# Optimization experiments

Measured on AMD Instinct MI355X. Metric: run time of the kernel, lower is better.

The kernel has to match this reference:

```python
import jax, jax.numpy as jnp
import numpy as np
import math

D = 300      # input_size
H = 5        # gat heads
NLAYERS = 2  # txt_gat_layer == img_gat_layer
N, L, K = 64, 1024, 64
E_TXT, E_IMG = 2048, 512


def _gat(x, edge_index, W, att_src, att_dst, bias):
    """PyG GATConv, concat=False (head mean), no self loops, eval mode (no dropout).
    x: (n, D); edge_index: (2, E); W: (D, H, D); att_*: (H, D); bias: (D,)."""
    n = x.shape[0]
    h = jnp.einsum('ld,dhe->lhe', x, W)                    # (n, H, D)
    src, dst = edge_index[0], edge_index[1]
    a_src = jnp.sum(h * att_src, axis=-1)                  # (n, H)
    a_dst = jnp.sum(h * att_dst, axis=-1)                  # (n, H)
    e = jax.nn.leaky_relu(a_src[src] + a_dst[dst], 0.2)    # (E, H)
    m = jax.ops.segment_max(e, dst, num_segments=n)        # per-target max
    m = jnp.where(jnp.isfinite(m), m, 0.0)                 # nodes w/o in-edges
    p = jnp.exp(e - m[dst])
    denom = jax.ops.segment_sum(p, dst, num_segments=n)
    alpha = p / (denom[dst] + 1e-16)                       # (E, H)
    out = jax.ops.segment_sum(alpha[:, :, None] * h[src], dst, num_segments=n)
    return out.mean(axis=1) + bias                         # (n, D)


def _layer_norm(x, g, b):
    mu = jnp.mean(x, axis=-1, keepdims=True)
    var = jnp.mean((x - mu) ** 2, axis=-1, keepdims=True)
    return (x - mu) / jnp.sqrt(var + 1e-5) * g + b


def _forward(t2, v2, score, edge_index, gnn_mask, key_padding_mask, np_mask,
             img_edge_index, txt_W, txt_att_src, txt_att_dst, txt_bias,
             img_W, img_att_src, img_att_dst, img_bias,
             w1, b1, w2, b2, ln_g, ln_b, lam=1.0):
    scale = 1.0 / jnp.sqrt(jnp.asarray(D, t2.dtype))
    q1 = jnp.einsum('nld,nkd->nlk', t2, v2) * scale        # (N, L, K)
    c = jnp.sum(score * t2, axis=1, keepdims=True)         # (N, 1, D)
    pa_token = t2 @ w1 + b1                                # (N, L)
    pa_token = jnp.where(key_padding_mask, -jnp.inf, pa_token)

    gat_txt = jax.vmap(_gat, in_axes=(0, 0, None, None, None, None))
    tnp = t2
    for i in range(NLAYERS):
        g = gat_txt(tnp, edge_index, txt_W[i], txt_att_src[i], txt_att_dst[i], txt_bias[i])
        g = jnp.where(gnn_mask[:, None, None], 0.0, g)     # masked graph -> zeros
        tnp = _layer_norm(jax.nn.relu(g), ln_g, ln_b)

    gat_img = jax.vmap(_gat, in_axes=(0, None, None, None, None, None))
    v3 = v2
    for i in range(NLAYERS):
        g = gat_img(v3, img_edge_index, img_W[i], img_att_src[i], img_att_dst[i], img_bias[i])
        v3 = _layer_norm(jax.nn.relu(g), ln_g, ln_b)

    tnp = jnp.concatenate([tnp, c], axis=1)                # (N, L+1, D)
    q2 = jnp.einsum('nld,nkd->nlk', tnp, v3) * scale       # (N, L+1, K)
    pa_np = tnp @ w2 + b2                                  # (N, L+1)
    pa_np = jnp.where(np_mask, -jnp.inf, pa_np)
    pa_np = jax.nn.softmax(pa_np * lam, axis=1)
    pa_tok = jax.nn.softmax(pa_token * lam, axis=1)
    a1 = jnp.sum(q1 * pa_tok[:, :, None], axis=1)          # (N, K)
    a2 = jnp.sum(q2 * pa_np[:, :, None], axis=1)           # (N, K)
    return jnp.concatenate([a1, a2], axis=1)               # (N, 2K)


def setup_inputs() -> dict:
    key = jax.random.key(0)
    ks = jax.random.split(key, 24)
    ws = 1.0 / math.sqrt(D)
    return {
        't2': jax.random.normal(ks[0], (N, L, D), jnp.float32),
        'v2': jax.random.normal(ks[1], (N, K, D), jnp.float32),
        'score': jax.random.uniform(ks[2], (N, L, D), jnp.float32),
        'edge_index': jax.random.randint(ks[3], (N, 2, E_TXT), 0, L),
        'gnn_mask': jnp.zeros((N,), bool),
        'key_padding_mask': jax.random.bernoulli(ks[4], 0.1, (N, L)),
        'np_mask': jax.random.bernoulli(ks[5], 0.1, (N, L + 1)),
        'img_edge_index': jax.random.randint(ks[6], (2, E_IMG), 0, K),
        'txt_W': jax.random.normal(ks[7], (NLAYERS, D, H, D), jnp.float32) * ws,
        'txt_att_src': jax.random.normal(ks[8], (NLAYERS, H, D), jnp.float32) * 0.1,
        'txt_att_dst': jax.random.normal(ks[9], (NLAYERS, H, D), jnp.float32) * 0.1,
        'txt_bias': jnp.zeros((NLAYERS, D), jnp.float32),
        'img_W': jax.random.normal(ks[10], (NLAYERS, D, H, D), jnp.float32) * ws,
        'img_att_src': jax.random.normal(ks[11], (NLAYERS, H, D), jnp.float32) * 0.1,
        'img_att_dst': jax.random.normal(ks[12], (NLAYERS, H, D), jnp.float32) * 0.1,
        'img_bias': jnp.zeros((NLAYERS, D), jnp.float32),
        'w1': jax.random.normal(ks[13], (D,), jnp.float32) * ws,
        'b1': jnp.zeros((), jnp.float32),
        'w2': jax.random.normal(ks[14], (D,), jnp.float32) * ws,
        'b2': jnp.zeros((), jnp.float32),
        'ln_g': jnp.ones((D,), jnp.float32),
        'ln_b': jnp.zeros((D,), jnp.float32),
    }


def reference(t2, v2, score, edge_index, gnn_mask, key_padding_mask, np_mask,
              img_edge_index, txt_W, txt_att_src, txt_att_dst, txt_bias,
              img_W, img_att_src, img_att_dst, img_bias,
              w1, b1, w2, b2, ln_g, ln_b):
    return _forward(t2, v2, score, edge_index, gnn_mask, key_padding_mask, np_mask,
                    img_edge_index, txt_W, txt_att_src, txt_att_dst, txt_bias,
                    img_W, img_att_src, img_att_dst, img_bias,
                    w1, b1, w2, b2, ln_g, ln_b)
```

## Files before the change

### kernel.cpp

```cpp
#include <hip/hip_runtime.h>
#include <hip/hip_bf16.h>
#include <math.h>

typedef __hip_bfloat16 bf16;
__device__ __forceinline__ float toF(float v){ return v; }
__device__ __forceinline__ float toF(bf16 v){ return __bfloat162float(v); }
__device__ __forceinline__ bf16 f2bf(float v){ return __float2bfloat16(v); }

#define D_    300
#define H_    5
#define NB    64
#define LL    1024
#define KK    64
#define ETXT  2048
#define EIMG  512
#define MAXDEG 128
#define KP    320
#define NP    1536

typedef __attribute__((ext_vector_type(8))) short short8;
typedef __attribute__((ext_vector_type(4))) float f32x4;

__device__ __forceinline__ int read_mask(const void* p, int i, int mode) {
  switch (mode) {
    case 1: return ((const unsigned short*)p)[i] != 0;
    case 2: return ((const unsigned char*)p)[i] != 0;
    case 3: { const unsigned int* w = (const unsigned int*)p;
              return (w[2*i] | w[2*i+1]) != 0; }
    default: return ((const unsigned int*)p)[i] != 0;
  }
}

__global__ void k_detect(const unsigned int* __restrict__ w, int nwords,
                         int* __restrict__ mode) {
  __shared__ unsigned int se[256], so[256];
  unsigned int oe = 0, oo = 0;
  for (int i = threadIdx.x; i < nwords; i += 256) {
    unsigned int v = w[i];
    if (i & 1) oo |= v; else oe |= v;
  }
  se[threadIdx.x] = oe; so[threadIdx.x] = oo;
  __syncthreads();
  for (int s = 128; s; s >>= 1) {
    if (threadIdx.x < s) { se[threadIdx.x] |= se[threadIdx.x+s]; so[threadIdx.x] |= so[threadIdx.x+s]; }
    __syncthreads();
  }
  if (threadIdx.x == 0) {
    unsigned int O = se[0] | so[0];
    int m = 0;
    if (O == 0u) m = 0;
    else if ((O & 0xFFFFu) == 0x3F80u) m = 1;
    else if ((O >> 16) == 0x3F80u && (O & 0xFFFFu) == 0u) m = 0;
    else if ((O >> 16) == 0x3FF0u) m = 3;
    else if (O <= 1u) m = (so[0] == 0u && se[0] != 0u) ? 3 : 0;
    else if ((O & 0xFEFEFEFEu) == 0u) m = 2;
    mode[0] = m;
  }
}

__global__ __launch_bounds__(256) void k_csr(const int* __restrict__ edges, int estride,
                                             int E, int nodes,
                                             int* __restrict__ rowptr, int rstride,
                                             int* __restrict__ col, int cstride) {
  int g = blockIdx.x, tid = threadIdx.x;
  __shared__ int cnt[1025];
  __shared__ int psum[257];
  const int* src = edges + (size_t)g * estride;
  const int* dst = src + E;
  for (int i = tid; i <= nodes; i += 256) cnt[i] = 0;
  __syncthreads();
  for (int e = tid; e < E; e += 256) atomicAdd(&cnt[dst[e]], 1);
  __syncthreads();
  int base = tid * 4;
  int loc = 0;
#pragma unroll
  for (int i = 0; i < 4; ++i) { int idx = base + i; if (idx < nodes) loc += cnt[idx]; }
  psum[tid + 1] = loc;
  if (tid == 0) psum[0] = 0;
  __syncthreads();
  if (tid == 0) { for (int i = 1; i <= 256; ++i) psum[i] += psum[i - 1]; }
  __syncthreads();
  int run = psum[tid];
  int starts[4];
#pragma unroll
  for (int i = 0; i < 4; ++i) {
    int idx = base + i;
    if (idx < nodes) { int c = cnt[idx]; starts[i] = run; run += c; }
  }
  __syncthreads();
#pragma unroll
  for (int i = 0; i < 4; ++i) {
    int idx = base + i;
    if (idx < nodes) { cnt[idx] = starts[i]; rowptr[(size_t)g * rstride + idx] = starts[i]; }
  }
  if (tid == 0) rowptr[(size_t)g * rstride + nodes] = E;
  __syncthreads();
  for (int e = tid; e < E; e += 256) {
    int pos = atomicAdd(&cnt[dst[e]], 1);
    col[(size_t)g * cstride + pos] = src[e];
  }
}

__global__ void k_c(const float* __restrict__ t2, const float* __restrict__ score,
                    float* __restrict__ c) {
  int n = blockIdx.x;
  int d = blockIdx.y * 128 + threadIdx.x;
  if (d >= D_) return;
  const float* tp = t2 + (size_t)n * LL * D_ + d;
  const float* sp = score + (size_t)n * LL * D_ + d;
  float acc = 0.f;
  for (int l = 0; l < LL; ++l)
    acc += tp[(size_t)l * D_] * sp[(size_t)l * D_];
  c[n * D_ + d] = acc;
}

__device__ __forceinline__ float clamp_logit(float v) {
  if (!(v > -1e30f)) v = -1e30f;
  if (v > 1e30f) v = 1e30f;
  return v;
}

__global__ void k_logits_tok(const float* __restrict__ x, const float* __restrict__ w,
                             const float* __restrict__ b, const void* __restrict__ mask,
                             const int* __restrict__ mmode,
                             float* __restrict__ logits, int rows) {
  int row = blockIdx.x * blockDim.y + threadIdx.y;
  if (row >= rows) return;
  int lane = threadIdx.x;
  const float* xp = x + (size_t)row * D_;
  float acc = 0.f;
  for (int d = lane; d < D_; d += 64) acc += xp[d] * w[d];
#pragma unroll
  for (int off = 32; off; off >>= 1) acc += __shfl_down(acc, off);
  if (lane == 0) {
    float v = clamp_logit(acc + b[0]);
    if (read_mask(mask, row, mmode[0])) v = -INFINITY;
    logits[row] = v;
  }
}

__global__ void k_logits_np(const bf16* __restrict__ X, const float* __restrict__ c,
                            const float* __restrict__ w, const float* __restrict__ b,
                            const void* __restrict__ mask, const int* __restrict__ mmode,
                            float* __restrict__ logits) {
  int row = blockIdx.x * blockDim.y + threadIdx.y;
  if (row >= NB * (LL + 1)) return;
  int n = row / (LL + 1), l = row % (LL + 1);
  int lane = threadIdx.x;
  float acc = 0.f;
  if (l < LL) {
    const bf16* xp = X + ((size_t)n * LL + l) * D_;
    for (int d = lane; d < D_; d += 64) acc += toF(xp[d]) * w[d];
  } else {
    const float* cp = c + n * D_;
    for (int d = lane; d < D_; d += 64) acc += cp[d] * w[d];
  }
#pragma unroll
  for (int off = 32; off; off >>= 1) acc += __shfl_down(acc, off);
  if (lane == 0) {
    float v = clamp_logit(acc + b[0]);
    if (read_mask(mask, row, mmode[0])) v = -INFINITY;
    logits[row] = v;
  }
}

__global__ __launch_bounds__(256) void k_soft_u1(const float* __restrict__ logits,
                                                 const float* __restrict__ t2,
                                                 float* __restrict__ u1) {
  int n = blockIdx.x, tid = threadIdx.x;
  __shared__ float w[LL];
  __shared__ float red[4];
  __shared__ float stat;
  float m = -INFINITY;
  for (int l = tid; l < LL; l += 256) { float v = logits[n * LL + l]; w[l] = v; m = fmaxf(m, v); }
#pragma unroll
  for (int off = 32; off; off >>= 1) m = fmaxf(m, __shfl_down(m, off));
  if ((tid & 63) == 0) red[tid >> 6] = m;
  __syncthreads();
  if (tid == 0) stat = fmaxf(fmaxf(red[0], red[1]), fmaxf(red[2], red[3]));
  __syncthreads();
  float M = stat;
  if (!(M > -INFINITY && M < INFINITY)) M = 0.f;
  float s = 0.f;
  for (int l = tid; l < LL; l += 256) { float p = __expf(w[l] - M); w[l] = p; s += p; }
#pragma unroll
  for (int off = 32; off; off >>= 1) s += __shfl_down(s, off);
  __syncthreads();
  if ((tid & 63) == 0) red[tid >> 6] = s;
  __syncthreads();
  if (tid == 0) stat = red[0] + red[1] + red[2] + red[3];
  __syncthreads();
  float inv = (stat > 0.f) ? 1.f / stat : 0.f;
  for (int d = tid; d < D_; d += 256) {
    float acc = 0.f;
    const float* tp = t2 + (size_t)n * LL * D_ + d;
    for (int l = 0; l < LL; ++l) acc += w[l] * tp[(size_t)l * D_];
    u1[n * D_ + d] = acc * inv;
  }
}

__global__ __launch_bounds__(256) void k_soft_u2(const float* __restrict__ logits,
                                                 const bf16* __restrict__ X,
                                                 const float* __restrict__ c,
                                                 float* __restrict__ u2) {
  int n = blockIdx.x, tid = threadIdx.x;
  __shared__ float w[LL + 1];
  __shared__ float red[4];
  __shared__ float stat;
  float m = -INFINITY;
  for (int l = tid; l < LL + 1; l += 256) { float v = logits[n * (LL + 1) + l]; w[l] = v; m = fmaxf(m, v); }
#pragma unroll
  for (int off = 32; off; off >>= 1) m = fmaxf(m, __shfl_down(m, off));
  if ((tid & 63) == 0) red[tid >> 6] = m;
  __syncthreads();
  if (tid == 0) stat = fmaxf(fmaxf(red[0], red[1]), fmaxf(red[2], red[3]));
  __syncthreads();
  float M = stat;
  if (!(M > -INFINITY && M < INFINITY)) M = 0.f;
  float s = 0.f;
  for (int l = tid; l < LL + 1; l += 256) { float p = __expf(w[l] - M); w[l] = p; s += p; }
#pragma unroll
  for (int off = 32; off; off >>= 1) s += __shfl_down(s, off);
  __syncthreads();
  if ((tid & 63) == 0) red[tid >> 6] = s;
  __syncthreads();
  if (tid == 0) stat = red[0] + red[1] + red[2] + red[3];
  __syncthreads();
  float inv = (stat > 0.f) ? 1.f / stat : 0.f;
  for (int d = tid; d < D_; d += 256) {
    float acc = 0.f;
    const bf16* xp = X + (size_t)n * LL * D_ + d;
    for (int l = 0; l < LL; ++l) acc += w[l] * toF(xp[(size_t)l * D_]);
    acc += w[LL] * c[n * D_ + d];
    u2[n * D_ + d] = acc * inv;
  }
}

__global__ void k_wvec(const float* __restrict__ W, const float* __restrict__ att_src,
                       const float* __restrict__ att_dst, float* __restrict__ wsrc,
                       float* __restrict__ wdst) {
  int idx = blockIdx.x * blockDim.x + threadIdx.x;
  if (idx >= 2 * H_ * D_) return;
  int s = idx / (H_ * D_);
  int r = idx % (H_ * D_);
  int h = r / D_, d = r % D_;
  const float* att = (s ? att_dst : att_src) + h * D_;
  const float* Wp = W + (size_t)d * H_ * D_ + h * D_;
  float acc = 0.f;
  for (int e = 0; e < D_; ++e) acc += Wp[e] * att[e];
  (s ? wdst : wsrc)[h * D_ + d] = acc;
}

template <typename T>
__global__ void k_asrc(const T* __restrict__ x, const float* __restrict__ wsrc,
                       const float* __restrict__ wdst, float* __restrict__ a_src,
                       float* __restrict__ a_dst, int rows) {
  int row = blockIdx.x * blockDim.y + threadIdx.y;
  if (row >= rows) return;
  int lane = threadIdx.x;
  const T* xp = x + (size_t)row * D_;
  float xr[5];
#pragma unroll
  for (int i = 0; i < 5; ++i) { int d = lane + 64 * i; xr[i] = (d < D_) ? toF(xp[d]) : 0.f; }
#pragma unroll
  for (int hh = 0; hh < H_; ++hh) {
    float as = 0.f, ad = 0.f;
#pragma unroll
    for (int i = 0; i < 5; ++i) {
      int d = lane + 64 * i;
      if (d < D_) { as += xr[i] * wsrc[hh * D_ + d]; ad += xr[i] * wdst[hh * D_ + d]; }
    }
#pragma unroll
    for (int off = 32; off; off >>= 1) { as += __shfl_down(as, off); ad += __shfl_down(ad, off); }
    if (lane == 0) { a_src[(size_t)row * H_ + hh] = as; a_dst[(size_t)row * H_ + hh] = ad; }
  }
}

template <typename T>
__global__ void k_packA(const T* __restrict__ src, bf16* __restrict__ Ap, int M) {
  int idx = blockIdx.x * 256 + threadIdx.x;
  if (idx >= M * KP) return;
  int m = idx / KP, k = idx - m * KP;
  Ap[idx] = (k < D_) ? f2bf(toF(src[(size_t)m * D_ + k])) : f2bf(0.f);
}

__global__ void k_packB(const float* __restrict__ B, bf16* __restrict__ Bp) {
  int idx = blockIdx.x * 256 + threadIdx.x;
  if (idx >= NP * KP) return;
  int j = idx / KP, k = idx - j * KP;
  float v = (k < D_ && j < H_ * D_) ? B[(size_t)k * (H_ * D_) + j] : 0.f;
  Bp[idx] = f2bf(v);
}

__global__ __launch_bounds__(256) void k_gemm_mfma(const bf16* __restrict__ Ap,
                                                   const bf16* __restrict__ Bp,
                                                   bf16* __restrict__ C, int M) {
  __shared__ short As[128][40];
  __shared__ short Bs[128][40];
  int m0 = blockIdx.x * 128, n0 = blockIdx.y * 128;
  int tid = threadIdx.x;
  int wave = tid >> 6, lane = tid & 63;
  int wr = (wave >> 1) * 64, wc = (wave & 1) * 64;
  f32x4 acc[4][4] = {};
  for (int k0 = 0; k0 < KP; k0 += 32) {
#pragma unroll
    for (int cc = 0; cc < 2; ++cc) {
      int c = tid + cc * 256;
      int m = c >> 2, ko = (c & 3) << 3;
      int row = m0 + m; if (row >= M) row = M - 1;
      *(uint4*)&As[m][ko] = *(const uint4*)(Ap + (size_t)row * KP + k0 + ko);
    }
#pragma unroll
    for (int cc = 0; cc < 2; ++cc) {
      int c = tid + cc * 256;
      int n = c >> 2, ko = (c & 3) << 3;
      *(uint4*)&Bs[n][ko] = *(const uint4*)(Bp + (size_t)(n0 + n) * KP + k0 + ko);
    }
    __syncthreads();
    int kq = (lane >> 4) << 3;
    short8 af[4], bfr[4];
#pragma unroll
    for (int i = 0; i < 4; ++i) af[i]  = *(const short8*)&As[wr + i * 16 + (lane & 15)][kq];
#pragma unroll
    for (int j = 0; j < 4; ++j) bfr[j] = *(const short8*)&Bs[wc + j * 16 + (lane & 15)][kq];
#pragma unroll
    for (int i = 0; i < 4; ++i)
#pragma unroll
      for (int j = 0; j < 4; ++j)
        acc[i][j] = __builtin_amdgcn_mfma_f32_16x16x32_bf16(af[i], bfr[j], acc[i][j], 0, 0, 0);
    __syncthreads();
  }
  int cl = lane & 15, rq = (lane >> 4) << 2;
#pragma unroll
  for (int i = 0; i < 4; ++i) {
#pragma unroll
    for (int j = 0; j < 4; ++j) {
      int col = n0 + wc + j * 16 + cl;
#pragma unroll
      for (int r = 0; r < 4; ++r) {
        int row = m0 + wr + i * 16 + rq + r;
        if (row < M) C[(size_t)row * NP + col] = f2bf(acc[i][j][r]);
      }
    }
  }
}

__global__ __launch_bounds__(256) void k_agg_ln(
    const bf16* __restrict__ h, const float* __restrict__ a_src, const float* __restrict__ a_dst,
    const int* __restrict__ rowptr, int rstride,
    const int* __restrict__ col, int cstride,
    int nodes, int lbpg, int swz, int gs,
    const void* __restrict__ gmask, const int* __restrict__ mmode, int g_off,
    const float* __restrict__ bias, const float* __restrict__ g_ln, const float* __restrict__ b_ln,
    bf16* __restrict__ xout) {
  int b = blockIdx.x;
  int wv = threadIdx.x >> 6, lane = threadIdx.x & 63;
  int g, nb;
  if (swz) { int j = b >> 3; g = (b & 7) + ((j >> lbpg) << 3); nb = j & ((1 << lbpg) - 1); }
  else     { g = b >> lbpg; nb = b & ((1 << lbpg) - 1); }
  int node = (nb << 2) + wv;
  if (g >= gs || node >= nodes) return;
  int gg = g_off + g;
  const int* rp = rowptr + (size_t)gg * rstride;
  int r0 = rp[node];
  int deg = rp[node + 1] - r0;
  if (deg > MAXDEG) deg = MAXDEG;
  const int* cp = col + (size_t)gg * cstride + r0;
  int row0 = g * nodes;
  const float* adr = a_dst + (size_t)(row0 + node) * H_;
  float ad[H_];
#pragma unroll
  for (int hh = 0; hh < H_; ++hh) ad[hh] = adr[hh];
  int d0 = deg < 64 ? deg : 64;
  int s0 = 0; float l0[H_];
  if (lane < d0) {
    s0 = cp[lane];
    const float* ap = a_src + (size_t)(row0 + s0) * H_;
#pragma unroll
    for (int hh = 0; hh < H_; ++hh) { float v = ap[hh] + ad[hh]; l0[hh] = v > 0.f ? v : 0.2f * v; }
  } else {
#pragma unroll
    for (int hh = 0; hh < H_; ++hh) l0[hh] = -INFINITY;
  }
  bool two = deg > 64;
  int s1 = 0; float l1[H_];
#pragma unroll
  for (int hh = 0; hh < H_; ++hh) l1[hh] = -INFINITY;
  if (two && lane < deg - 64) {
    s1 = cp[64 + lane];
    const float* ap = a_src + (size_t)(row0 + s1) * H_;
#pragma unroll
    for (int hh = 0; hh < H_; ++hh) { float v = ap[hh] + ad[hh]; l1[hh] = v > 0.f ? v : 0.2f * v; }
  }
  float al0[H_], al1[H_];
#pragma unroll
  for (int hh = 0; hh < H_; ++hh) {
    float m = two ? fmaxf(l0[hh], l1[hh]) : l0[hh];
    for (int off = 1; off < deg && off < 64; off <<= 1) m = fmaxf(m, __shfl_xor(m, off));
    m = __shfl(m, 0);
    float e0 = (lane < d0) ? __expf(l0[hh] - m) : 0.f;
    float e1 = (two && lane < deg - 64) ? __expf(l1[hh] - m) : 0.f;
    float s = e0 + e1;
    for (int off = 1; off < deg && off < 64; off <<= 1) s += __shfl_xor(s, off);
    s = __shfl(s, 0);
    float inv = 1.f / (s + 1e-16f);
    al0[hh] = e0 * inv;
    al1[hh] = e1 * inv;
  }
  float acc[3][2] = {};
  const char* hb = (const char*)h;
  for (int i = 0; i < deg; ++i) {
    int si; float aw[H_];
    if (i < 64) {
      si = __shfl(s0, i);
#pragma unroll
      for (int hh = 0; hh < H_; ++hh) aw[hh] = __shfl(al0[hh], i);
    } else {
      si = __shfl(s1, i - 64);
#pragma unroll
      for (int hh = 0; hh < H_; ++hh) aw[hh] = __shfl(al1[hh], i - 64);
    }
    const char* rb = hb + (size_t)(row0 + si) * (NP * 2);
#pragma unroll
    for (int t = 0; t < 3; ++t) {
      int d2 = lane + 64 * t;
      if (d2 < 150) {
#pragma unroll
        for (int hh = 0; hh < H_; ++hh) {
          unsigned int u = *(const unsigned int*)(rb + hh * (D_ * 2) + d2 * 4);
          float lo = __uint_as_float(u << 16);
          float hi = __uint_as_float(u & 0xFFFF0000u);
          acc[t][0] += aw[hh] * lo;
          acc[t][1] += aw[hh] * hi;
        }
      }
    }
  }
  int msk = gmask ? read_mask(gmask, gg, mmode[0]) : 0;
  float y[3][2];
  float ps = 0.f, pq = 0.f;
#pragma unroll
  for (int t = 0; t < 3; ++t) {
    int d2 = lane + 64 * t;
    float y0 = 0.f, y1 = 0.f;
    if (d2 < 150) {
      float2 bb = *(const float2*)&bias[d2 * 2];
      y0 = acc[t][0] * (1.f / H_) + bb.x;
      y1 = acc[t][1] * (1.f / H_) + bb.y;
      if (msk) { y0 = 0.f; y1 = 0.f; }
      y0 = fmaxf(y0, 0.f); y1 = fmaxf(y1, 0.f);
      ps += y0 + y1; pq += y0 * y0 + y1 * y1;
    }
    y[t][0] = y0; y[t][1] = y1;
  }
#pragma unroll
  for (int off = 1; off < 64; off <<= 1) { ps += __shfl_xor(ps, off); pq += __shfl_xor(pq, off); }
  float mu = ps * (1.f / 300.f);
  float var = pq * (1.f / 300.f) - mu * mu;
  var = fmaxf(var, 0.f);
  float rstd = rsqrtf(var + 1e-5f);
  char* orow = (char*)(xout + (size_t)(row0 + node) * D_);
#pragma unroll
  for (int t = 0; t < 3; ++t) {
    int d2 = lane + 64 * t;
    if (d2 < 150) {
      float2 gv = *(const float2*)&g_ln[d2 * 2];
      float2 bv = *(const float2*)&b_ln[d2 * 2];
      float o0 = (y[t][0] - mu) * rstd * gv.x + bv.x;
      float o1 = (y[t][1] - mu) * rstd * gv.y + bv.y;
      bf16 c0 = f2bf(o0), c1 = f2bf(o1);
      unsigned int u = ((unsigned int)*(unsigned short*)&c1 << 16) | (unsigned int)*(unsigned short*)&c0;
      *(unsigned int*)(orow + d2 * 4) = u;
    }
  }
}

__global__ void k_out(const float* __restrict__ u1, const float* __restrict__ u2,
                      const float* __restrict__ v2, const bf16* __restrict__ v3,
                      float* __restrict__ out) {
  int idx = blockIdx.x * blockDim.y + threadIdx.y;
  if (idx >= NB * KK) return;
  int n = idx / KK, k = idx - n * KK;
  int lane = threadIdx.x;
  const float* ap = v2 + (size_t)idx * D_;
  const bf16* bp = v3 + (size_t)idx * D_;
  const float* u1p = u1 + n * D_;
  const float* u2p = u2 + n * D_;
  float a1 = 0.f, a2 = 0.f;
  for (int d = lane; d < D_; d += 64) { a1 += u1p[d] * ap[d]; a2 += u2p[d] * toF(bp[d]); }
#pragma unroll
  for (int off = 32; off; off >>= 1) { a1 += __shfl_down(a1, off); a2 += __shfl_down(a2, off); }
  if (lane == 0) {
    const float scale = 0.05773502691896258f;
    out[(size_t)n * 2 * KK + k] = a1 * scale;
    out[(size_t)n * 2 * KK + KK + k] = a2 * scale;
  }
}

extern "C" void kernel_launch(void* const* d_in, const int* in_sizes, int n_in,
                              void* d_out, int out_size, void* d_ws, size_t ws_size,
                              hipStream_t stream) {
  const float* t2    = (const float*)d_in[0];
  const float* v2    = (const float*)d_in[1];
  const float* score = (const float*)d_in[2];
  const int*   eidx  = (const int*)d_in[3];
  const void*  gmask = d_in[4];
  const void*  kpm   = d_in[5];
  const void*  npm   = d_in[6];
  const int*   iedge = (const int*)d_in[7];
  const float* txtW  = (const float*)d_in[8];
  const float* txtAs = (const float*)d_in[9];
  const float* txtAd = (const float*)d_in[10];
  const float* txtB  = (const float*)d_in[11];
  const float* imgW  = (const float*)d_in[12];
  const float* imgAs = (const float*)d_in[13];
  const float* imgAd = (const float*)d_in[14];
  const float* imgB  = (const float*)d_in[15];
  const float* w1    = (const float*)d_in[16];
  const float* b1    = (const float*)d_in[17];
  const float* w2    = (const float*)d_in[18];
  const float* b2    = (const float*)d_in[19];
  const float* lng   = (const float*)d_in[20];
  const float* lnb   = (const float*)d_in[21];
  float* out = (float*)d_out;

  char* ws = (char*)d_ws;
  size_t off = 0;
  auto alloc = [&](size_t bytes) -> char* {
    char* p = ws + off;
    off += (bytes + 511) & ~(size_t)511;
    return p;
  };
  int*   mmode = (int*)alloc(64);
  float* c    = (float*)alloc((size_t)NB * D_ * 4);
  float* u1   = (float*)alloc((size_t)NB * D_ * 4);
  float* u2   = (float*)alloc((size_t)NB * D_ * 4);
  float* lg1  = (float*)alloc((size_t)NB * LL * 4);
  float* lg2  = (float*)alloc((size_t)NB * (LL + 1) * 4);
  float* wsrc = (float*)alloc((size_t)H_ * D_ * 4);
  float* wdst = (float*)alloc((size_t)H_ * D_ * 4);
  float* asrc = (float*)alloc((size_t)NB * LL * H_ * 4);
  float* adst = (float*)alloc((size_t)NB * LL * H_ * 4);
  int*   trp  = (int*)alloc((size_t)NB * (LL + 1) * 4);
  int*   tcol = (int*)alloc((size_t)NB * ETXT * 4);
  int*   irp  = (int*)alloc((size_t)(KK + 1) * 4);
  int*   icol = (int*)alloc((size_t)EIMG * 4);
  bf16* X  = (bf16*)alloc((size_t)NB * LL * D_ * 2);
  bf16* V  = (bf16*)alloc((size_t)NB * KK * D_ * 2);
  bf16* Bp = (bf16*)alloc((size_t)NP * KP * 2);
  size_t havail = (ws_size > off) ? (ws_size - off) : 0;
  char* hstart = ws + off;
  size_t per_g_txt = (size_t)LL * (KP + NP) * 2;
  int cg = (int)(havail / per_g_txt);
  if (cg < 1) cg = 1;
  if (cg > NB) cg = NB;
  size_t per_g_img = (size_t)KK * (KP + NP) * 2;
  int cgi = (int)(havail / per_g_img);
  if (cgi < 1) cgi = 1;
  if (cgi > NB) cgi = NB;

  dim3 b64x4(64, 4);

  k_detect<<<1, 256, 0, stream>>>((const unsigned int*)kpm, NB * LL / 4, mmode);

  k_csr<<<NB, 256, 0, stream>>>(eidx, 2 * ETXT, ETXT, LL, trp, LL + 1, tcol, ETXT);
  k_csr<<<1, 256, 0, stream>>>(iedge, 0, EIMG, KK, irp, 0, icol, 0);

  k_c<<<dim3(NB, 3), 128, 0, stream>>>(t2, score, c);
  k_logits_tok<<<(NB * LL + 3) / 4, b64x4, 0, stream>>>(t2, w1, b1, kpm, mmode, lg1, NB * LL);
  k_soft_u1<<<NB, 256, 0, stream>>>(lg1, t2, u1);

  {
    bf16* Ap   = (bf16*)hstart;
    bf16* hbuf = (bf16*)(hstart + (size_t)cg * LL * KP * 2);
    for (int layer = 0; layer < 2; ++layer) {
      const float* W = txtW + (size_t)layer * D_ * H_ * D_;
      k_packB<<<(NP * KP + 255) / 256, 256, 0, stream>>>(W, Bp);
      k_wvec<<<(2 * H_ * D_ + 255) / 256, 256, 0, stream>>>(
          W, txtAs + layer * H_ * D_, txtAd + layer * H_ * D_, wsrc, wdst);
      for (int g0 = 0; g0 < NB; g0 += cg) {
        int gs = (cg < NB - g0) ? cg : (NB - g0);
        int M = gs * LL;
        bf16* Xout = X + (size_t)g0 * LL * D_;
        if (layer == 0) {
          const float* Xin = t2 + (size_t)g0 * LL * D_;
          k_packA<float><<<(M * KP + 255) / 256, 256, 0, stream>>>(Xin, Ap, M);
          k_asrc<float><<<(M + 3) / 4, b64x4, 0, stream>>>(Xin, wsrc, wdst, asrc, adst, M);
        } else {
          const bf16* Xin = X + (size_t)g0 * LL * D_;
          k_packA<bf16><<<(M * KP + 255) / 256, 256, 0, stream>>>(Xin, Ap, M);
          k_asrc<bf16><<<(M + 3) / 4, b64x4, 0, stream>>>(Xin, wsrc, wdst, asrc, adst, M);
        }
        k_gemm_mfma<<<dim3((M + 127) / 128, NP / 128), 256, 0, stream>>>(Ap, Bp, hbuf, M);
        int swz = (gs % 8 == 0);
        k_agg_ln<<<gs * (LL / 4), 256, 0, stream>>>(hbuf, asrc, adst, trp, LL + 1, tcol, ETXT,
                                                    LL, 8, swz, gs, gmask, mmode, g0,
                                                    txtB + layer * D_, lng, lnb, Xout);
      }
    }
  }

  {
    bf16* Ap   = (bf16*)hstart;
    bf16* hbuf = (bf16*)(hstart + (size_t)cgi * KK * KP * 2);
    for (int layer = 0; layer < 2; ++layer) {
      const float* W = imgW + (size_t)layer * D_ * H_ * D_;
      k_packB<<<(NP * KP + 255) / 256, 256, 0, stream>>>(W, Bp);
      k_wvec<<<(2 * H_ * D_ + 255) / 256, 256, 0, stream>>>(
          W, imgAs + layer * H_ * D_, imgAd + layer * H_ * D_, wsrc, wdst);
      for (int g0 = 0; g0 < NB; g0 += cgi) {
        int gs = (cgi < NB - g0) ? cgi : (NB - g0);
        int M = gs * KK;
        bf16* Vout = V + (size_t)g0 * KK * D_;
        if (layer == 0) {
          const float* Vin = v2 + (size_t)g0 * KK * D_;
          k_packA<float><<<(M * KP + 255) / 256, 256, 0, stream>>>(Vin, Ap, M);
          k_asrc<float><<<(M + 3) / 4, b64x4, 0, stream>>>(Vin, wsrc, wdst, asrc, adst, M);
        } else {
          const bf16* Vin = V + (size_t)g0 * KK * D_;
          k_packA<bf16><<<(M * KP + 255) / 256, 256, 0, stream>>>(Vin, Ap, M);
          k_asrc<bf16><<<(M + 3) / 4, b64x4, 0, stream>>>(Vin, wsrc, wdst, asrc, adst, M);
        }
        k_gemm_mfma<<<dim3((M + 127) / 128, NP / 128), 256, 0, stream>>>(Ap, Bp, hbuf, M);
        int swz = (gs % 8 == 0);
        k_agg_ln<<<gs * (KK / 4), 256, 0, stream>>>(hbuf, asrc, adst, irp, 0, icol, 0,
                                                    KK, 4, swz, gs, nullptr, mmode, 0,
                                                    imgB + layer * D_, lng, lnb, Vout);
      }
    }
  }

  k_logits_np<<<(NB * (LL + 1) + 3) / 4, b64x4, 0, stream>>>(X, c, w2, b2, npm, mmode, lg2);
  k_soft_u2<<<NB, 256, 0, stream>>>(lg2, X, c, u2);
  k_out<<<(NB * KK + 3) / 4, b64x4, 0, stream>>>(u1, u2, v2, V, out);
}
```

Before: 1.189 ms.

## Aggregate inputs before projection, fuse head-mean into GEMM, split softmax-pooling reductions

The GAT layer is reordered so each node first aggregates its neighbours' raw inputs per head (Z, width H*D). A single GEMM against the head-averaged, repacked weight then produces the output directly with bias, mask, ReLU and LayerNorm fused in. This replaces the projection to the full H*D hidden tensor followed by aggregation. The c and u1/u2 reductions are split into per-l partial sums over a 4-way grid with 1024-thread blocks, and softmax weights are computed in a separate kernel. bf16 loads are vectorised as packed pairs. This cuts the wide GEMM output traffic and fixes low parallelism in the per-batch reduction kernels, at the cost of more kernel launches and a larger K dimension in the GEMM.

```diff
diff --git a/kernel.cpp b/kernel.cpp
--- a/kernel.cpp
+++ b/kernel.cpp
@@ -15,8 +15,9 @@
 #define ETXT  2048
 #define EIMG  512
 #define MAXDEG 128
-#define KP    320
-#define NP    1536
+#define KC    1504
+#define BN2   320
+#define BM2   64
 
 typedef __attribute__((ext_vector_type(8))) short short8;
 typedef __attribute__((ext_vector_type(4))) float f32x4;
@@ -101,17 +102,36 @@
   }
 }
 
-__global__ void k_c(const float* __restrict__ t2, const float* __restrict__ score,
-                    float* __restrict__ c) {
-  int n = blockIdx.x;
-  int d = blockIdx.y * 128 + threadIdx.x;
-  if (d >= D_) return;
-  const float* tp = t2 + (size_t)n * LL * D_ + d;
-  const float* sp = score + (size_t)n * LL * D_ + d;
-  float acc = 0.f;
-  for (int l = 0; l < LL; ++l)
-    acc += tp[(size_t)l * D_] * sp[(size_t)l * D_];
-  c[n * D_ + d] = acc;
+__global__ __launch_bounds__(1024) void k_c_part(const float* __restrict__ t2,
+                                                 const float* __restrict__ score,
+                                                 float* __restrict__ cpart) {
+  int n = blockIdx.x, part = blockIdx.y;
+  int lane = threadIdx.x & 63, ty = threadIdx.x >> 6;
+  __shared__ float red[16][304];
+  float acc[5] = {0.f, 0.f, 0.f, 0.f, 0.f};
+  int l0 = part * 256;
+  for (int l = l0 + ty; l < l0 + 256; l += 16) {
+    const float* tp = t2 + ((size_t)n * LL + l) * D_;
+    const float* sp = score + ((size_t)n * LL + l) * D_;
+#pragma unroll
+    for (int j = 0; j < 5; ++j) { int d = lane + 64 * j; if (d < D_) acc[j] += tp[d] * sp[d]; }
+  }
+#pragma unroll
+  for (int j = 0; j < 5; ++j) { int d = lane + 64 * j; if (d < D_) red[ty][d] = acc[j]; }
+  __syncthreads();
+  for (int d = threadIdx.x; d < D_; d += 1024) {
+    float s = 0.f;
+#pragma unroll
+    for (int t = 0; t < 16; ++t) s += red[t][d];
+    cpart[((size_t)part * NB + n) * D_ + d] = s;
+  }
+}
+
+__global__ void k_c_red(const float* __restrict__ cpart, float* __restrict__ c) {
+  int idx = blockIdx.x * 256 + threadIdx.x;
+  if (idx >= NB * D_) return;
+  const int S = NB * D_;
+  c[idx] = cpart[idx] + cpart[S + idx] + cpart[2 * S + idx] + cpart[3 * S + idx];
 }
 
 __device__ __forceinline__ float clamp_logit(float v) {
@@ -149,8 +169,16 @@
   int lane = threadIdx.x;
   float acc = 0.f;
   if (l < LL) {
-    const bf16* xp = X + ((size_t)n * LL + l) * D_;
-    for (int d = lane; d < D_; d += 64) acc += toF(xp[d]) * w[d];
+    const char* xp = (const char*)(X + ((size_t)n * LL + l) * D_);
+#pragma unroll
+    for (int t = 0; t < 3; ++t) {
+      int d2 = lane + 64 * t;
+      if (d2 < 150) {
+        unsigned int u = *(const unsigned int*)(xp + d2 * 4);
+        float2 wv = *(const float2*)&w[d2 * 2];
+        acc += __uint_as_float(u << 16) * wv.x + __uint_as_float(u & 0xFFFF0000u) * wv.y;
+      }
+    }
   } else {
     const float* cp = c + n * D_;
     for (int d = lane; d < D_; d += 64) acc += cp[d] * w[d];
@@ -164,76 +192,121 @@
   }
 }
 
-__global__ __launch_bounds__(256) void k_soft_u1(const float* __restrict__ logits,
-                                                 const float* __restrict__ t2,
-                                                 float* __restrict__ u1) {
-  int n = blockIdx.x, tid = threadIdx.x;
-  __shared__ float w[LL];
-  __shared__ float red[4];
+__global__ __launch_bounds__(1024) void k_pa(const float* __restrict__ lg1,
+                                             const float* __restrict__ lg2,
+                                             float* __restrict__ pa1,
+                                             float* __restrict__ pa2) {
+  int b = blockIdx.x, tid = threadIdx.x;
+  int which = b >> 6, n = b & 63;
+  const float* lg = which ? (lg2 + (size_t)n * (LL + 1)) : (lg1 + (size_t)n * LL);
+  float* pa = which ? (pa2 + (size_t)n * (LL + 1)) : (pa1 + (size_t)n * LL);
+  __shared__ float red[16];
   __shared__ float stat;
-  float m = -INFINITY;
-  for (int l = tid; l < LL; l += 256) { float v = logits[n * LL + l]; w[l] = v; m = fmaxf(m, v); }
-#pragma unroll
-  for (int off = 32; off; off >>= 1) m = fmaxf(m, __shfl_down(m, off));
+  float v0 = lg[tid];
+  float vx = (which && tid == 0) ? lg[LL] : -INFINITY;
+  float m = fmaxf(v0, vx);
+#pragma unroll
+  for (int off = 32; off; off >>= 1) m = fmaxf(m, __shfl_xor(m, off));
   if ((tid & 63) == 0) red[tid >> 6] = m;
   __syncthreads();
-  if (tid == 0) stat = fmaxf(fmaxf(red[0], red[1]), fmaxf(red[2], red[3]));
+  if (tid == 0) {
+    float mm = red[0];
+    for (int i = 1; i < 16; ++i) mm = fmaxf(mm, red[i]);
+    stat = mm;
+  }
   __syncthreads();
   float M = stat;
   if (!(M > -INFINITY && M < INFINITY)) M = 0.f;
-  float s = 0.f;
-  for (int l = tid; l < LL; l += 256) { float p = __expf(w[l] - M); w[l] = p; s += p; }
-#pragma unroll
-  for (int off = 32; off; off >>= 1) s += __shfl_down(s, off);
+  float p0 = __expf(v0 - M);
+  float px = (which && tid == 0) ? __expf(vx - M) : 0.f;
+  float s = p0 + px;
+#pragma unroll
+  for (int off = 32; off; off >>= 1) s += __shfl_xor(s, off);
   __syncthreads();
   if ((tid & 63) == 0) red[tid >> 6] = s;
   __syncthreads();
-  if (tid == 0) stat = red[0] + red[1] + red[2] + red[3];
+  if (tid == 0) {
+    float ss = 0.f;
+    for (int i = 0; i < 16; ++i) ss += red[i];
+    stat = ss;
+  }
   __syncthreads();
   float inv = (stat > 0.f) ? 1.f / stat : 0.f;
-  for (int d = tid; d < D_; d += 256) {
-    float acc = 0.f;
-    const float* tp = t2 + (size_t)n * LL * D_ + d;
-    for (int l = 0; l < LL; ++l) acc += w[l] * tp[(size_t)l * D_];
-    u1[n * D_ + d] = acc * inv;
-  }
-}
-
-__global__ __launch_bounds__(256) void k_soft_u2(const float* __restrict__ logits,
+  pa[tid] = p0 * inv;
+  if (which && tid == 0) pa[LL] = px * inv;
+}
+
+__global__ __launch_bounds__(1024) void k_u1part(const float* __restrict__ pa1,
+                                                 const float* __restrict__ t2,
+                                                 float* __restrict__ up) {
+  int n = blockIdx.x, part = blockIdx.y;
+  int lane = threadIdx.x & 63, ty = threadIdx.x >> 6;
+  __shared__ float red[16][304];
+  float acc[5] = {0.f, 0.f, 0.f, 0.f, 0.f};
+  const float* pw = pa1 + (size_t)n * LL;
+  int l0 = part * 256;
+  for (int l = l0 + ty; l < l0 + 256; l += 16) {
+    float w = pw[l];
+    const float* tp = t2 + ((size_t)n * LL + l) * D_;
+#pragma unroll
+    for (int j = 0; j < 5; ++j) { int d = lane + 64 * j; if (d < D_) acc[j] += w * tp[d]; }
+  }
+#pragma unroll
+  for (int j = 0; j < 5; ++j) { int d = lane + 64 * j; if (d < D_) red[ty][d] = acc[j]; }
+  __syncthreads();
+  for (int d = threadIdx.x; d < D_; d += 1024) {
+    float s = 0.f;
+#pragma unroll
+    for (int t = 0; t < 16; ++t) s += red[t][d];
+    up[((size_t)part * NB + n) * D_ + d] = s;
+  }
+}
+
+__global__ __launch_bounds__(1024) void k_u2part(const float* __restrict__ pa2,
                                                  const bf16* __restrict__ X,
                                                  const float* __restrict__ c,
-                                                 float* __restrict__ u2) {
-  int n = blockIdx.x, tid = threadIdx.x;
-  __shared__ float w[LL + 1];
-  __shared__ float red[4];
-  __shared__ float stat;
-  float m = -INFINITY;
-  for (int l = tid; l < LL + 1; l += 256) { float v = logits[n * (LL + 1) + l]; w[l] = v; m = fmaxf(m, v); }
-#pragma unroll
-  for (int off = 32; off; off >>= 1) m = fmaxf(m, __shfl_down(m, off));
-  if ((tid & 63) == 0) red[tid >> 6] = m;
-  __syncthreads();
-  if (tid == 0) stat = fmaxf(fmaxf(red[0], red[1]), fmaxf(red[2], red[3]));
-  __syncthreads();
-  float M = stat;
-  if (!(M > -INFINITY && M < INFINITY)) M = 0.f;
-  float s = 0.f;
-  for (int l = tid; l < LL + 1; l += 256) { float p = __expf(w[l] - M); w[l] = p; s += p; }
-#pragma unroll
-  for (int off = 32; off; off >>= 1) s += __shfl_down(s, off);
-  __syncthreads();
-  if ((tid & 63) == 0) red[tid >> 6] = s;
-  __syncthreads();
-  if (tid == 0) stat = red[0] + red[1] + red[2] + red[3];
-  __syncthreads();
-  float inv = (stat > 0.f) ? 1.f / stat : 0.f;
-  for (int d = tid; d < D_; d += 256) {
-    float acc = 0.f;
-    const bf16* xp = X + (size_t)n * LL * D_ + d;
-    for (int l = 0; l < LL; ++l) acc += w[l] * toF(xp[(size_t)l * D_]);
-    acc += w[LL] * c[n * D_ + d];
-    u2[n * D_ + d] = acc * inv;
-  }
+                                                 float* __restrict__ up) {
+  int n = blockIdx.x, part = blockIdx.y;
+  int lane = threadIdx.x & 63, ty = threadIdx.x >> 6;
+  __shared__ float red[16][304];
+  float acc[3][2] = {};
+  const float* pw = pa2 + (size_t)n * (LL + 1);
+  int l0 = part * 256;
+  for (int l = l0 + ty; l < l0 + 256; l += 16) {
+    float w = pw[l];
+    const char* xp = (const char*)(X + ((size_t)n * LL + l) * D_);
+#pragma unroll
+    for (int t = 0; t < 3; ++t) {
+      int d2 = lane + 64 * t;
+      if (d2 < 150) {
+        unsigned int u = *(const unsigned int*)(xp + d2 * 4);
+        acc[t][0] += w * __uint_as_float(u << 16);
+        acc[t][1] += w * __uint_as_float(u & 0xFFFF0000u);
+      }
+    }
+  }
+#pragma unroll
+  for (int t = 0; t < 3; ++t) {
+    int d2 = lane + 64 * t;
+    if (d2 < 150) { red[ty][d2 * 2] = acc[t][0]; red[ty][d2 * 2 + 1] = acc[t][1]; }
+  }
+  __syncthreads();
+  for (int d = threadIdx.x; d < D_; d += 1024) {
+    float s = 0.f;
+#pragma unroll
+    for (int t = 0; t < 16; ++t) s += red[t][d];
+    if (part == 3) s += pw[LL] * c[(size_t)n * D_ + d];
+    up[((size_t)part * NB + n) * D_ + d] = s;
+  }
+}
+
+__global__ void k_ured(const float* __restrict__ up1, const float* __restrict__ up2,
+                       float* __restrict__ u1, float* __restrict__ u2) {
+  int idx = blockIdx.x * 256 + threadIdx.x;
+  if (idx >= NB * D_) return;
+  const int S = NB * D_;
+  u1[idx] = up1[idx] + up1[S + idx] + up1[2 * S + idx] + up1[3 * S + idx];
+  u2[idx] = up2[idx] + up2[S + idx] + up2[2 * S + idx] + up2[3 * S + idx];
 }
 
 __global__ void k_wvec(const float* __restrict__ W, const float* __restrict__ att_src,
@@ -258,17 +331,32 @@
   int row = blockIdx.x * blockDim.y + threadIdx.y;
   if (row >= rows) return;
   int lane = threadIdx.x;
-  const T* xp = x + (size_t)row * D_;
-  float xr[5];
-#pragma unroll
-  for (int i = 0; i < 5; ++i) { int d = lane + 64 * i; xr[i] = (d < D_) ? toF(xp[d]) : 0.f; }
+  float xr[3][2];
+#pragma unroll
+  for (int t = 0; t < 3; ++t) {
+    int d2 = lane + 64 * t;
+    if (d2 < 150) {
+      if constexpr (sizeof(T) == 4) {
+        float2 v = *(const float2*)((const float*)x + (size_t)row * D_ + d2 * 2);
+        xr[t][0] = v.x; xr[t][1] = v.y;
+      } else {
+        unsigned int u = *(const unsigned int*)((const char*)x + ((size_t)row * D_) * 2 + d2 * 4);
+        xr[t][0] = __uint_as_float(u << 16); xr[t][1] = __uint_as_float(u & 0xFFFF0000u);
+      }
+    } else { xr[t][0] = 0.f; xr[t][1] = 0.f; }
+  }
 #pragma unroll
   for (int hh = 0; hh < H_; ++hh) {
     float as = 0.f, ad = 0.f;
 #pragma unroll
-    for (int i = 0; i < 5; ++i) {
-      int d = lane + 64 * i;
-      if (d < D_) { as += xr[i] * wsrc[hh * D_ + d]; ad += xr[i] * wdst[hh * D_ + d]; }
+    for (int t = 0; t < 3; ++t) {
+      int d2 = lane + 64 * t;
+      if (d2 < 150) {
+        float2 ws = *(const float2*)&wsrc[hh * D_ + d2 * 2];
+        float2 wd = *(const float2*)&wdst[hh * D_ + d2 * 2];
+        as += xr[t][0] * ws.x + xr[t][1] * ws.y;
+        ad += xr[t][0] * wd.x + xr[t][1] * wd.y;
+      }
     }
 #pragma unroll
     for (int off = 32; off; off >>= 1) { as += __shfl_down(as, off); ad += __shfl_down(ad, off); }
@@ -276,83 +364,25 @@
   }
 }
 
+__global__ void k_packWc(const float* __restrict__ W, bf16* __restrict__ Wcp) {
+  int idx = blockIdx.x * 256 + threadIdx.x;
+  if (idx >= BN2 * KC) return;
+  int j = idx / KC, k = idx - j * KC;
+  float v = 0.f;
+  if (j < D_ && k < H_ * D_) {
+    int h = k / D_, e = k - h * D_;
+    v = W[(size_t)e * (H_ * D_) + h * D_ + j] * (1.f / H_);
+  }
+  Wcp[idx] = f2bf(v);
+}
+
 template <typename T>
-__global__ void k_packA(const T* __restrict__ src, bf16* __restrict__ Ap, int M) {
-  int idx = blockIdx.x * 256 + threadIdx.x;
-  if (idx >= M * KP) return;
-  int m = idx / KP, k = idx - m * KP;
-  Ap[idx] = (k < D_) ? f2bf(toF(src[(size_t)m * D_ + k])) : f2bf(0.f);
-}
-
-__global__ void k_packB(const float* __restrict__ B, bf16* __restrict__ Bp) {
-  int idx = blockIdx.x * 256 + threadIdx.x;
-  if (idx >= NP * KP) return;
-  int j = idx / KP, k = idx - j * KP;
-  float v = (k < D_ && j < H_ * D_) ? B[(size_t)k * (H_ * D_) + j] : 0.f;
-  Bp[idx] = f2bf(v);
-}
-
-__global__ __launch_bounds__(256) void k_gemm_mfma(const bf16* __restrict__ Ap,
-                                                   const bf16* __restrict__ Bp,
-                                                   bf16* __restrict__ C, int M) {
-  __shared__ short As[128][40];
-  __shared__ short Bs[128][40];
-  int m0 = blockIdx.x * 128, n0 = blockIdx.y * 128;
-  int tid = threadIdx.x;
-  int wave = tid >> 6, lane = tid & 63;
-  int wr = (wave >> 1) * 64, wc = (wave & 1) * 64;
-  f32x4 acc[4][4] = {};
-  for (int k0 = 0; k0 < KP; k0 += 32) {
-#pragma unroll
-    for (int cc = 0; cc < 2; ++cc) {
-      int c = tid + cc * 256;
-      int m = c >> 2, ko = (c & 3) << 3;
-      int row = m0 + m; if (row >= M) row = M - 1;
-      *(uint4*)&As[m][ko] = *(const uint4*)(Ap + (size_t)row * KP + k0 + ko);
-    }
-#pragma unroll
-    for (int cc = 0; cc < 2; ++cc) {
-      int c = tid + cc * 256;
-      int n = c >> 2, ko = (c & 3) << 3;
-      *(uint4*)&Bs[n][ko] = *(const uint4*)(Bp + (size_t)(n0 + n) * KP + k0 + ko);
-    }
-    __syncthreads();
-    int kq = (lane >> 4) << 3;
-    short8 af[4], bfr[4];
-#pragma unroll
-    for (int i = 0; i < 4; ++i) af[i]  = *(const short8*)&As[wr + i * 16 + (lane & 15)][kq];
-#pragma unroll
-    for (int j = 0; j < 4; ++j) bfr[j] = *(const short8*)&Bs[wc + j * 16 + (lane & 15)][kq];
-#pragma unroll
-    for (int i = 0; i < 4; ++i)
-#pragma unroll
-      for (int j = 0; j < 4; ++j)
-        acc[i][j] = __builtin_amdgcn_mfma_f32_16x16x32_bf16(af[i], bfr[j], acc[i][j], 0, 0, 0);
-    __syncthreads();
-  }
-  int cl = lane & 15, rq = (lane >> 4) << 2;
-#pragma unroll
-  for (int i = 0; i < 4; ++i) {
-#pragma unroll
-    for (int j = 0; j < 4; ++j) {
-      int col = n0 + wc + j * 16 + cl;
-#pragma unroll
-      for (int r = 0; r < 4; ++r) {
-        int row = m0 + wr + i * 16 + rq + r;
-        if (row < M) C[(size_t)row * NP + col] = f2bf(acc[i][j][r]);
-      }
-    }
-  }
-}
-
-__global__ __launch_bounds__(256) void k_agg_ln(
-    const bf16* __restrict__ h, const float* __restrict__ a_src, const float* __restrict__ a_dst,
+__global__ __launch_bounds__(256) void k_aggx(
+    const T* __restrict__ x, const float* __restrict__ a_src, const float* __restrict__ a_dst,
     const int* __restrict__ rowptr, int rstride,
     const int* __restrict__ col, int cstride,
-    int nodes, int lbpg, int swz, int gs,
-    const void* __restrict__ gmask, const int* __restrict__ mmode, int g_off,
-    const float* __restrict__ bias, const float* __restrict__ g_ln, const float* __restrict__ b_ln,
-    bf16* __restrict__ xout) {
+    int nodes, int lbpg, int swz, int gs, int g_off,
+    bf16* __restrict__ Z) {
   int b = blockIdx.x;
   int wv = threadIdx.x >> 6, lane = threadIdx.x & 63;
   int g, nb;
@@ -407,8 +437,7 @@
     al0[hh] = e0 * inv;
     al1[hh] = e1 * inv;
   }
-  float acc[3][2] = {};
-  const char* hb = (const char*)h;
+  float acc[H_][3][2] = {};
   for (int i = 0; i < deg; ++i) {
     int si; float aw[H_];
     if (i < 64) {
@@ -420,58 +449,154 @@
 #pragma unroll
       for (int hh = 0; hh < H_; ++hh) aw[hh] = __shfl(al1[hh], i - 64);
     }
-    const char* rb = hb + (size_t)(row0 + si) * (NP * 2);
 #pragma unroll
     for (int t = 0; t < 3; ++t) {
       int d2 = lane + 64 * t;
       if (d2 < 150) {
-#pragma unroll
-        for (int hh = 0; hh < H_; ++hh) {
-          unsigned int u = *(const unsigned int*)(rb + hh * (D_ * 2) + d2 * 4);
-          float lo = __uint_as_float(u << 16);
-          float hi = __uint_as_float(u & 0xFFFF0000u);
-          acc[t][0] += aw[hh] * lo;
-          acc[t][1] += aw[hh] * hi;
+        float lo, hi;
+        if constexpr (sizeof(T) == 4) {
+          float2 v = *(const float2*)((const float*)x + (size_t)(row0 + si) * D_ + d2 * 2);
+          lo = v.x; hi = v.y;
+        } else {
+          unsigned int u = *(const unsigned int*)((const char*)x + ((size_t)(row0 + si) * D_) * 2 + d2 * 4);
+          lo = __uint_as_float(u << 16); hi = __uint_as_float(u & 0xFFFF0000u);
         }
-      }
-    }
-  }
-  int msk = gmask ? read_mask(gmask, gg, mmode[0]) : 0;
-  float y[3][2];
-  float ps = 0.f, pq = 0.f;
-#pragma unroll
-  for (int t = 0; t < 3; ++t) {
-    int d2 = lane + 64 * t;
-    float y0 = 0.f, y1 = 0.f;
-    if (d2 < 150) {
-      float2 bb = *(const float2*)&bias[d2 * 2];
-      y0 = acc[t][0] * (1.f / H_) + bb.x;
-      y1 = acc[t][1] * (1.f / H_) + bb.y;
-      if (msk) { y0 = 0.f; y1 = 0.f; }
-      y0 = fmaxf(y0, 0.f); y1 = fmaxf(y1, 0.f);
-      ps += y0 + y1; pq += y0 * y0 + y1 * y1;
-    }
-    y[t][0] = y0; y[t][1] = y1;
-  }
-#pragma unroll
-  for (int off = 1; off < 64; off <<= 1) { ps += __shfl_xor(ps, off); pq += __shfl_xor(pq, off); }
-  float mu = ps * (1.f / 300.f);
-  float var = pq * (1.f / 300.f) - mu * mu;
-  var = fmaxf(var, 0.f);
-  float rstd = rsqrtf(var + 1e-5f);
-  char* orow = (char*)(xout + (size_t)(row0 + node) * D_);
-#pragma unroll
-  for (int t = 0; t < 3; ++t) {
-    int d2 = lane + 64 * t;
-    if (d2 < 150) {
-      float2 gv = *(const float2*)&g_ln[d2 * 2];
-      float2 bv = *(const float2*)&b_ln[d2 * 2];
-      float o0 = (y[t][0] - mu) * rstd * gv.x + bv.x;
-      float o1 = (y[t][1] - mu) * rstd * gv.y + bv.y;
-      bf16 c0 = f2bf(o0), c1 = f2bf(o1);
-      unsigned int u = ((unsigned int)*(unsigned short*)&c1 << 16) | (unsigned int)*(unsigned short*)&c0;
-      *(unsigned int*)(orow + d2 * 4) = u;
-    }
+#pragma unroll
+        for (int hh = 0; hh < H_; ++hh) { acc[hh][t][0] += aw[hh] * lo; acc[hh][t][1] += aw[hh] * hi; }
+      }
+    }
+  }
+  char* zr = (char*)(Z + (size_t)(row0 + node) * KC);
+#pragma unroll
+  for (int hh = 0; hh < H_; ++hh)
+#pragma unroll
+    for (int t = 0; t < 3; ++t) {
+      int d2 = lane + 64 * t;
+      if (d2 < 150) {
+        bf16 c0 = f2bf(acc[hh][t][0]), c1 = f2bf(acc[hh][t][1]);
+        unsigned int u = ((unsigned int)*(unsigned short*)&c1 << 16) | (unsigned int)*(unsigned short*)&c0;
+        *(unsigned int*)(zr + (hh * 300 + d2 * 2) * 2) = u;
+      }
+    }
+  if (lane < 2) *(unsigned int*)(zr + 3000 + lane * 4) = 0u;
+}
+
+union SmemU {
+  struct { short As[BM2][40]; short Bs[BN2][40]; } s;
+  unsigned short Osh[64][304];
+};
+
+__global__ __launch_bounds__(256) void k_gemm2(
+    const bf16* __restrict__ Z, const bf16* __restrict__ Wcp,
+    const float* __restrict__ bias,
+    const void* __restrict__ gmask, const int* __restrict__ mmode, int g_off, int nodes,
+    const float* __restrict__ g_ln, const float* __restrict__ b_ln,
+    bf16* __restrict__ xout) {
+  __shared__ SmemU u;
+  __shared__ float sS[4][64], sQ[4][64];
+  __shared__ float sMu[64], sRs[64];
+  int tid = threadIdx.x;
+  int wave = tid >> 6, lane = tid & 63;
+  int cl = lane & 15, qw = lane >> 4;
+  int brow = blockIdx.x * BM2;
+  const bf16* Zb = Z + (size_t)brow * KC;
+  f32x4 acc[4][5] = {};
+  for (int k0 = 0; k0 < KC; k0 += 32) {
+    { int r = tid >> 2, ko = (tid & 3) << 3;
+      *(uint4*)&u.s.As[r][ko] = *(const uint4*)(Zb + (size_t)r * KC + k0 + ko); }
+    for (int cjob = tid; cjob < 1280; cjob += 256) {
+      int r = cjob >> 2, ko = (cjob & 3) << 3;
+      *(uint4*)&u.s.Bs[r][ko] = *(const uint4*)(Wcp + (size_t)r * KC + k0 + ko);
+    }
+    __syncthreads();
+    int kq = qw << 3;
+    short8 af[4], bfr[5];
+#pragma unroll
+    for (int i = 0; i < 4; ++i) af[i] = *(const short8*)&u.s.As[i * 16 + cl][kq];
+#pragma unroll
+    for (int j = 0; j < 5; ++j) bfr[j] = *(const short8*)&u.s.Bs[wave * 80 + j * 16 + cl][kq];
+#pragma unroll
+    for (int i = 0; i < 4; ++i)
+#pragma unroll
+      for (int j = 0; j < 5; ++j)
+        acc[i][j] = __builtin_amdgcn_mfma_f32_16x16x32_bf16(af[i], bfr[j], acc[i][j], 0, 0, 0);
+    __syncthreads();
+  }
+  int msk = gmask ? read_mask(gmask, g_off + brow / nodes, mmode[0]) : 0;
+  float rs[4][4], rq[4][4];
+#pragma unroll
+  for (int i = 0; i < 4; ++i)
+#pragma unroll
+    for (int r = 0; r < 4; ++r) { rs[i][r] = 0.f; rq[i][r] = 0.f; }
+#pragma unroll
+  for (int i = 0; i < 4; ++i)
+#pragma unroll
+    for (int j = 0; j < 5; ++j) {
+      int colc = wave * 80 + j * 16 + cl;
+      bool cv = colc < D_;
+      float bb = cv ? bias[colc] : 0.f;
+#pragma unroll
+      for (int r = 0; r < 4; ++r) {
+        float y = acc[i][j][r] + bb;
+        if (msk) y = 0.f;
+        y = fmaxf(y, 0.f);
+        if (!cv) y = 0.f;
+        acc[i][j][r] = y;
+        rs[i][r] += y;
+        rq[i][r] += y * y;
+      }
+    }
+#pragma unroll
+  for (int off = 1; off < 16; off <<= 1) {
+#pragma unroll
+    for (int i = 0; i < 4; ++i)
+#pragma unroll
+      for (int r = 0; r < 4; ++r) {
+        rs[i][r] += __shfl_xor(rs[i][r], off);
+        rq[i][r] += __shfl_xor(rq[i][r], off);
+      }
+  }
+  if (cl == 0) {
+#pragma unroll
+    for (int i = 0; i < 4; ++i)
+#pragma unroll
+      for (int r = 0; r < 4; ++r) {
+        sS[wave][i * 16 + qw * 4 + r] = rs[i][r];
+        sQ[wave][i * 16 + qw * 4 + r] = rq[i][r];
+      }
+  }
+  __syncthreads();
+  if (tid < 64) {
+    float s = sS[0][tid] + sS[1][tid] + sS[2][tid] + sS[3][tid];
+    float q = sQ[0][tid] + sQ[1][tid] + sQ[2][tid] + sQ[3][tid];
+    float mu = s * (1.f / 300.f);
+    float var = q * (1.f / 300.f) - mu * mu;
+    var = fmaxf(var, 0.f);
+    sMu[tid] = mu;
+    sRs[tid] = rsqrtf(var + 1e-5f);
+  }
+  __syncthreads();
+#pragma unroll
+  for (int i = 0; i < 4; ++i)
+#pragma unroll
+    for (int j = 0; j < 5; ++j) {
+      int colc = wave * 80 + j * 16 + cl;
+      if (colc < D_) {
+        float gv = g_ln[colc], bv = b_ln[colc];
+#pragma unroll
+        for (int r = 0; r < 4; ++r) {
+          int row = i * 16 + qw * 4 + r;
+          float o = (acc[i][j][r] - sMu[row]) * sRs[row] * gv + bv;
+          bf16 cb = f2bf(o);
+          u.Osh[row][colc] = *(unsigned short*)&cb;
+        }
+      }
+    }
+  __syncthreads();
+  char* ob = (char*)(xout + (size_t)brow * D_);
+  for (int idx = tid; idx < 64 * 150; idx += 256) {
+    int r = idx / 150, c2 = idx - r * 150;
+    *(unsigned int*)(ob + (size_t)r * 600 + c2 * 4) = *(const unsigned int*)&u.Osh[r][c2 * 2];
   }
 }
 
@@ -532,29 +657,34 @@
     return p;
   };
   int*   mmode = (int*)alloc(64);
-  float* c    = (float*)alloc((size_t)NB * D_ * 4);
-  float* u1   = (float*)alloc((size_t)NB * D_ * 4);
-  float* u2   = (float*)alloc((size_t)NB * D_ * 4);
-  float* lg1  = (float*)alloc((size_t)NB * LL * 4);
-  float* lg2  = (float*)alloc((size_t)NB * (LL + 1) * 4);
-  float* wsrc = (float*)alloc((size_t)H_ * D_ * 4);
-  float* wdst = (float*)alloc((size_t)H_ * D_ * 4);
-  float* asrc = (float*)alloc((size_t)NB * LL * H_ * 4);
-  float* adst = (float*)alloc((size_t)NB * LL * H_ * 4);
-  int*   trp  = (int*)alloc((size_t)NB * (LL + 1) * 4);
-  int*   tcol = (int*)alloc((size_t)NB * ETXT * 4);
-  int*   irp  = (int*)alloc((size_t)(KK + 1) * 4);
-  int*   icol = (int*)alloc((size_t)EIMG * 4);
-  bf16* X  = (bf16*)alloc((size_t)NB * LL * D_ * 2);
-  bf16* V  = (bf16*)alloc((size_t)NB * KK * D_ * 2);
-  bf16* Bp = (bf16*)alloc((size_t)NP * KP * 2);
+  float* c     = (float*)alloc((size_t)NB * D_ * 4);
+  float* u1    = (float*)alloc((size_t)NB * D_ * 4);
+  float* u2    = (float*)alloc((size_t)NB * D_ * 4);
+  float* lg1   = (float*)alloc((size_t)NB * LL * 4);
+  float* lg2   = (float*)alloc((size_t)NB * (LL + 1) * 4);
+  float* pa1   = (float*)alloc((size_t)NB * LL * 4);
+  float* pa2   = (float*)alloc((size_t)NB * (LL + 1) * 4);
+  float* cpart = (float*)alloc((size_t)4 * NB * D_ * 4);
+  float* up1   = (float*)alloc((size_t)4 * NB * D_ * 4);
+  float* up2   = (float*)alloc((size_t)4 * NB * D_ * 4);
+  float* wsrc  = (float*)alloc((size_t)H_ * D_ * 4);
+  float* wdst  = (float*)alloc((size_t)H_ * D_ * 4);
+  float* asrc  = (float*)alloc((size_t)NB * LL * H_ * 4);
+  float* adst  = (float*)alloc((size_t)NB * LL * H_ * 4);
+  int*   trp   = (int*)alloc((size_t)NB * (LL + 1) * 4);
+  int*   tcol  = (int*)alloc((size_t)NB * ETXT * 4);
+  int*   irp   = (int*)alloc((size_t)(KK + 1) * 4);
+  int*   icol  = (int*)alloc((size_t)EIMG * 4);
+  bf16*  X     = (bf16*)alloc((size_t)NB * LL * D_ * 2);
+  bf16*  V     = (bf16*)alloc((size_t)NB * KK * D_ * 2);
+  bf16*  Wcp   = (bf16*)alloc((size_t)BN2 * KC * 2);
   size_t havail = (ws_size > off) ? (ws_size - off) : 0;
-  char* hstart = ws + off;
-  size_t per_g_txt = (size_t)LL * (KP + NP) * 2;
+  bf16* Z = (bf16*)(ws + off);
+  size_t per_g_txt = (size_t)LL * KC * 2;
   int cg = (int)(havail / per_g_txt);
   if (cg < 1) cg = 1;
   if (cg > NB) cg = NB;
-  size_t per_g_img = (size_t)KK * (KP + NP) * 2;
+  size_t per_g_img = (size_t)KK * KC * 2;
   int cgi = (int)(havail / per_g_img);
   if (cgi < 1) cgi = 1;
   if (cgi > NB) cgi = NB;
@@ -566,71 +696,66 @@
   k_csr<<<NB, 256, 0, stream>>>(eidx, 2 * ETXT, ETXT, LL, trp, LL + 1, tcol, ETXT);
   k_csr<<<1, 256, 0, stream>>>(iedge, 0, EIMG, KK, irp, 0, icol, 0);
 
-  k_c<<<dim3(NB, 3), 128, 0, stream>>>(t2, score, c);
+  k_c_part<<<dim3(NB, 4), 1024, 0, stream>>>(t2, score, cpart);
+  k_c_red<<<(NB * D_ + 255) / 256, 256, 0, stream>>>(cpart, c);
   k_logits_tok<<<(NB * LL + 3) / 4, b64x4, 0, stream>>>(t2, w1, b1, kpm, mmode, lg1, NB * LL);
-  k_soft_u1<<<NB, 256, 0, stream>>>(lg1, t2, u1);
-
-  {
-    bf16* Ap   = (bf16*)hstart;
-    bf16* hbuf = (bf16*)(hstart + (size_t)cg * LL * KP * 2);
-    for (int layer = 0; layer < 2; ++layer) {
-      const float* W = txtW + (size_t)layer * D_ * H_ * D_;
-      k_packB<<<(NP * KP + 255) / 256, 256, 0, stream>>>(W, Bp);
-      k_wvec<<<(2 * H_ * D_ + 255) / 256, 256, 0, stream>>>(
-          W, txtAs + layer * H_ * D_, txtAd + layer * H_ * D_, wsrc, wdst);
-      for (int g0 = 0; g0 < NB; g0 += cg) {
-        int gs = (cg < NB - g0) ? cg : (NB - g0);
-        int M = gs * LL;
-        bf16* Xout = X + (size_t)g0 * LL * D_;
-        if (layer == 0) {
-          const float* Xin = t2 + (size_t)g0 * LL * D_;
-          k_packA<float><<<(M * KP + 255) / 256, 256, 0, stream>>>(Xin, Ap, M);
-          k_asrc<float><<<(M + 3) / 4, b64x4, 0, stream>>>(Xin, wsrc, wdst, asrc, adst, M);
-        } else {
-          const bf16* Xin = X + (size_t)g0 * LL * D_;
-          k_packA<bf16><<<(M * KP + 255) / 256, 256, 0, stream>>>(Xin, Ap, M);
-          k_asrc<bf16><<<(M + 3) / 4, b64x4, 0, stream>>>(Xin, wsrc, wdst, asrc, adst, M);
-        }
-        k_gemm_mfma<<<dim3((M + 127) / 128, NP / 128), 256, 0, stream>>>(Ap, Bp, hbuf, M);
-        int swz = (gs % 8 == 0);
-        k_agg_ln<<<gs * (LL / 4), 256, 0, stream>>>(hbuf, asrc, adst, trp, LL + 1, tcol, ETXT,
-                                                    LL, 8, swz, gs, gmask, mmode, g0,
-                                                    txtB + layer * D_, lng, lnb, Xout);
-      }
-    }
-  }
-
-  {
-    bf16* Ap   = (bf16*)hstart;
-    bf16* hbuf = (bf16*)(hstart + (size_t)cgi * KK * KP * 2);
-    for (int layer = 0; layer < 2; ++layer) {
-      const float* W = imgW + (size_t)layer * D_ * H_ * D_;
-      k_packB<<<(NP * KP + 255) / 256, 256, 0, stream>>>(W, Bp);
-      k_wvec<<<(2 * H_ * D_ + 255) / 256, 256, 0, stream>>>(
-          W, imgAs + layer * H_ * D_, imgAd + layer * H_ * D_, wsrc, wdst);
-      for (int g0 = 0; g0 < NB; g0 += cgi) {
-        int gs = (cgi < NB - g0) ? cgi : (NB - g0);
-        int M = gs * KK;
-        bf16* Vout = V + (size_t)g0 * KK * D_;
-        if (layer == 0) {
-          const float* Vin = v2 + (size_t)g0 * KK * D_;
-          k_packA<float><<<(M * KP + 255) / 256, 256, 0, stream>>>(Vin, Ap, M);
-          k_asrc<float><<<(M + 3) / 4, b64x4, 0, stream>>>(Vin, wsrc, wdst, asrc, adst, M);
-        } else {
-          const bf16* Vin = V + (size_t)g0 * KK * D_;
-          k_packA<bf16><<<(M * KP + 255) / 256, 256, 0, stream>>>(Vin, Ap, M);
-          k_asrc<bf16><<<(M + 3) / 4, b64x4, 0, stream>>>(Vin, wsrc, wdst, asrc, adst, M);
-        }
-        k_gemm_mfma<<<dim3((M + 127) / 128, NP / 128), 256, 0, stream>>>(Ap, Bp, hbuf, M);
-        int swz = (gs % 8 == 0);
-        k_agg_ln<<<gs * (KK / 4), 256, 0, stream>>>(hbuf, asrc, adst, irp, 0, icol, 0,
-                                                    KK, 4, swz, gs, nullptr, mmode, 0,
-                                                    imgB + layer * D_, lng, lnb, Vout);
-      }
+
+  for (int layer = 0; layer < 2; ++layer) {
+    const float* W = txtW + (size_t)layer * D_ * H_ * D_;
+    k_packWc<<<(BN2 * KC + 255) / 256, 256, 0, stream>>>(W, Wcp);
+    k_wvec<<<(2 * H_ * D_ + 255) / 256, 256, 0, stream>>>(
+        W, txtAs + layer * H_ * D_, txtAd + layer * H_ * D_, wsrc, wdst);
+    for (int g0 = 0; g0 < NB; g0 += cg) {
+      int gs = (cg < NB - g0) ? cg : (NB - g0);
+      int M = gs * LL;
+      int swz = (gs % 8 == 0);
+      bf16* Xout = X + (size_t)g0 * LL * D_;
+      if (layer == 0) {
+        const float* Xin = t2 + (size_t)g0 * LL * D_;
+        k_asrc<float><<<(M + 3) / 4, b64x4, 0, stream>>>(Xin, wsrc, wdst, asrc, adst, M);
+        k_aggx<float><<<gs * (LL / 4), 256, 0, stream>>>(Xin, asrc, adst, trp, LL + 1, tcol, ETXT,
+                                                         LL, 8, swz, gs, g0, Z);
+      } else {
+        const bf16* Xin = X + (size_t)g0 * LL * D_;
+        k_asrc<bf16><<<(M + 3) / 4, b64x4, 0, stream>>>(Xin, wsrc, wdst, asrc, adst, M);
+        k_aggx<bf16><<<gs * (LL / 4), 256, 0, stream>>>(Xin, asrc, adst, trp, LL + 1, tcol, ETXT,
+                                                        LL, 8, swz, gs, g0, Z);
+      }
+      k_gemm2<<<M / BM2, 256, 0, stream>>>(Z, Wcp, txtB + layer * D_, gmask, mmode, g0, LL,
+                                           lng, lnb, Xout);
+    }
+  }
+
+  for (int layer = 0; layer < 2; ++layer) {
+    const float* W = imgW + (size_t)layer * D_ * H_ * D_;
+    k_packWc<<<(BN2 * KC + 255) / 256, 256, 0, stream>>>(W, Wcp);
+    k_wvec<<<(2 * H_ * D_ + 255) / 256, 256, 0, stream>>>(
+        W, imgAs + layer * H_ * D_, imgAd + layer * H_ * D_, wsrc, wdst);
+    for (int g0 = 0; g0 < NB; g0 += cgi) {
+      int gs = (cgi < NB - g0) ? cgi : (NB - g0);
+      int M = gs * KK;
+      int swz = (gs % 8 == 0);
+      bf16* Vout = V + (size_t)g0 * KK * D_;
+      if (layer == 0) {
+        const float* Vin = v2 + (size_t)g0 * KK * D_;
+        k_asrc<float><<<(M + 3) / 4, b64x4, 0, stream>>>(Vin, wsrc, wdst, asrc, adst, M);
+        k_aggx<float><<<gs * (KK / 4), 256, 0, stream>>>(Vin, asrc, adst, irp, 0, icol, 0,
+                                                         KK, 4, swz, gs, 0, Z);
+      } else {
+        const bf16* Vin = V + (size_t)g0 * KK * D_;
+        k_asrc<bf16><<<(M + 3) / 4, b64x4, 0, stream>>>(Vin, wsrc, wdst, asrc, adst, M);
+        k_aggx<bf16><<<gs * (KK / 4), 256, 0, stream>>>(Vin, asrc, adst, irp, 0, icol, 0,
+                                                        KK, 4, swz, gs, 0, Z);
+      }
+      k_gemm2<<<M / BM2, 256, 0, stream>>>(Z, Wcp, imgB + layer * D_, nullptr, mmode, 0, KK,
+                                           lng, lnb, Vout);
     }
   }
 
   k_logits_np<<<(NB * (LL + 1) + 3) / 4, b64x4, 0, stream>>>(X, c, w2, b2, npm, mmode, lg2);
-  k_soft_u2<<<NB, 256, 0, stream>>>(lg2, X, c, u2);
+  k_pa<<<128, 1024, 0, stream>>>(lg1, lg2, pa1, pa2);
+  k_u1part<<<dim3(NB, 4), 1024, 0, stream>>>(pa1, t2, up1);
+  k_u2part<<<dim3(NB, 4), 1024, 0, stream>>>(pa2, X, c, up2);
+  k_ured<<<(NB * D_ + 255) / 256, 256, 0, stream>>>(up1, up2, u1, u2);
   k_out<<<(NB * KK + 3) / 4, b64x4, 0, stream>>>(u1, u2, v2, V, out);
 }
```

Result: slower. 1.456 ms (+22.4%).
